# Optimization experiments

Measured on AMD Instinct MI355X. Metric: run time of the kernel, lower is better.

The kernel has to match this reference:

```python
import jax, jax.numpy as jnp
import numpy as np

B, P, D, F = 2048, 16, 1024, 512  # batch, n_prompt, dim, fusion_dim
S = 2 * P  # sequence length
H = D // 2  # classifier hidden
LN_EPS = 1e-5


def _ln_relu(y, g, b):
    mu = jnp.mean(y, axis=-1, keepdims=True)
    var = jnp.mean(jnp.square(y - mu), axis=-1, keepdims=True)
    return jax.nn.relu((y - mu) * jax.lax.rsqrt(var + LN_EPS) * g + b)


def setup_inputs() -> dict:
    key = jax.random.key(0)
    ks = jax.random.split(key, 24)
    n = lambda k, shp, scale: jax.random.normal(k, shp, dtype=jnp.float32) * scale
    return {
        "q": n(ks[0], (B, S, D), 1.0),
        # nn.MultiheadAttention (1 head, batch_first)
        "in_proj_w": n(ks[1], (3 * D, D), 1.0 / np.sqrt(D)),
        "in_proj_b": jnp.zeros((3 * D,), jnp.float32),
        "out_w": n(ks[2], (D, D), 1.0 / np.sqrt(D)),
        "out_b": jnp.zeros((D,), jnp.float32),
        # 32 per-position classifiers, stacked: Linear(D,H)+ReLU+Linear(H,1)+ReLU
        "cls_w1": n(ks[3], (S, H, D), 1.0 / np.sqrt(D)),
        "cls_b1": jnp.zeros((S, H), jnp.float32),
        "cls_w2": n(ks[4], (S, H), 1.0 / np.sqrt(H)),
        "cls_b2": jnp.zeros((S,), jnp.float32),
        # fusion / projector heads: Linear(D,F)+LayerNorm(F)+ReLU
        "fus_w": n(ks[5], (F, D), 1.0 / np.sqrt(D)),
        "fus_b": jnp.zeros((F,), jnp.float32),
        "fus_g": jnp.ones((F,), jnp.float32),
        "fus_be": jnp.zeros((F,), jnp.float32),
        "pa_w": n(ks[6], (F, D), 1.0 / np.sqrt(D)),
        "pa_b": jnp.zeros((F,), jnp.float32),
        "pa_g": jnp.ones((F,), jnp.float32),
        "pa_be": jnp.zeros((F,), jnp.float32),
        "pv_w": n(ks[7], (F, D), 1.0 / np.sqrt(D)),
        "pv_b": jnp.zeros((F,), jnp.float32),
        "pv_g": jnp.ones((F,), jnp.float32),
        "pv_be": jnp.zeros((F,), jnp.float32),
    }


def reference(q, in_proj_w, in_proj_b, out_w, out_b,
              cls_w1, cls_b1, cls_w2, cls_b2,
              fus_w, fus_b, fus_g, fus_be,
              pa_w, pa_b, pa_g, pa_be,
              pv_w, pv_b, pv_g, pv_be):
    # --- single-head self-attention (nn.MultiheadAttention, eval mode) ---
    wq, wk, wv = jnp.split(in_proj_w, 3, axis=0)
    bq, bk, bv = jnp.split(in_proj_b, 3, axis=0)
    qp = jnp.einsum('bsd,ed->bse', q, wq) + bq
    kp = jnp.einsum('bsd,ed->bse', q, wk) + bk
    vp = jnp.einsum('bsd,ed->bse', q, wv) + bv
    scores = jnp.einsum('bse,bte->bst', qp, kp) / jnp.sqrt(jnp.float32(D))
    attn = jax.nn.softmax(scores, axis=-1)
    q_att = jnp.einsum('bst,bte->bse', attn, vp)
    q_att = jnp.einsum('bse,de->bsd', q_att, out_w) + out_b

    # --- per-position tiny classifiers, batched over the 32 slots ---
    h = jax.nn.relu(jnp.einsum('bsd,shd->bsh', q, cls_w1) + cls_b1)  # [B,S,H]
    d = jax.nn.relu(jnp.einsum('bsh,sh->bs', h, cls_w2) + cls_b2)    # [B,S]

    d_a = jax.nn.softmax(d[:, :P], axis=-1)
    d_v = jax.nn.softmax(d[:, P:], axis=-1)
    audio = jnp.einsum('bsd,bs->bd', q_att[:, :P, :], d_a)
    video = jnp.einsum('bsd,bs->bd', q_att[:, P:, :], d_v)
    fusion = (audio + video) * 0.5

    fusion_h = _ln_relu(fusion @ fus_w.T + fus_b, fus_g, fus_be)
    fusion_a = _ln_relu(audio @ pa_w.T + pa_b, pa_g, pa_be)
    fusion_v = _ln_relu(video @ pv_w.T + pv_b, pv_g, pv_be)
    return (fusion_h, fusion_a, fusion_v, d_a, d_v)
```

## Files before the change

kernel.cpp:

```cpp
#include <hip/hip_runtime.h>

#define Bdim 2048
#define Sdim 32
#define Ddim 1024
#define Fdim 512
#define Hdim 512

typedef __bf16 bf16_t;
typedef __bf16 bf16x8 __attribute__((ext_vector_type(8)));
typedef __bf16 bf16x4 __attribute__((ext_vector_type(4)));
typedef float  f32x4  __attribute__((ext_vector_type(4)));

#define BM 128
#define BN 128
#define BK 32

__device__ __forceinline__ void gll16(const bf16_t* g, bf16_t* l) {
  __builtin_amdgcn_global_load_lds((const __attribute__((address_space(1))) void*)g,
                                   (__attribute__((address_space(3))) void*)l,
                                   16, 0, 0);
}

__global__ void k_cvt(const float* __restrict__ s, bf16_t* __restrict__ d, long n) {
  long i = ((long)blockIdx.x * blockDim.x + threadIdx.x) * 4;
  long stride = (long)gridDim.x * blockDim.x * 4;
  for (; i < n; i += stride) {
    float4 v = *(const float4*)(s + i);
    bf16x4 o;
    o[0] = (bf16_t)v.x; o[1] = (bf16_t)v.y; o[2] = (bf16_t)v.z; o[3] = (bf16_t)v.w;
    *(bf16x4*)(d + i) = o;
  }
}

__global__ void k_bias_pre(const float* __restrict__ ipw, const float* __restrict__ ipb,
                           const float* __restrict__ ow, const float* __restrict__ ob,
                           float* __restrict__ u, float* __restrict__ w,
                           float* __restrict__ bp, float* __restrict__ c0) {
  int blk = blockIdx.x, tid = threadIdx.x;
  if (blk < 4) {
    int d = blk * 256 + tid;
    float acc = 0.f;
    for (int e = 0; e < Ddim; ++e) acc += ipw[(long)e * Ddim + d] * ipb[Ddim + e];
    u[d] = acc;
  } else if (blk < 8) {
    int d = (blk - 4) * 256 + tid;
    float acc = 0.f;
    for (int e = 0; e < Ddim; ++e) acc += ipw[(long)(Ddim + e) * Ddim + d] * ipb[e];
    w[d] = acc;
  } else if (blk < 136) {
    int o = (blk - 8) * 8 + (tid >> 5);
    int l = tid & 31;
    float acc = 0.f;
    for (int e = l; e < Ddim; e += 32) acc += ow[(long)o * Ddim + e] * ipb[2 * Ddim + e];
    #pragma unroll
    for (int m = 1; m < 32; m <<= 1) acc += __shfl_xor(acc, m);
    if (l == 0) bp[o] = acc + ob[o];
  } else {
    __shared__ float red[256];
    float acc = 0.f;
    for (int e = tid; e < Ddim; e += 256) acc += ipb[e] * ipb[Ddim + e];
    red[tid] = acc;
    __syncthreads();
    for (int off = 128; off; off >>= 1) {
      if (tid < off) red[tid] += red[tid + off];
      __syncthreads();
    }
    if (tid == 0) c0[0] = red[0];
  }
}

template<int AT, int BT>
__device__ __forceinline__ void gemm_tile(const bf16_t* __restrict__ A, long lda,
                                          const bf16_t* __restrict__ Bt, long ldb,
                                          long m0, long n0, int K,
                                          bf16_t* sa, bf16_t* sb, f32x4 acc[4][4]) {
  const int tid  = threadIdx.x;
  const int wave = tid >> 6;
  const int lane = tid & 63;
  const int quad = lane >> 4;
  const int l16  = lane & 15;
  const int wm = (wave & 1) * 64;
  const int wn = (wave >> 1) * 64;

  for (int kt = 0; kt < K; kt += BK) {
    __syncthreads();
    if constexpr (AT == 0) {
      #pragma unroll
      for (int r = 0; r < 2; ++r) {
        int L = r * 256 + tid;
        const bf16_t* g = A + (m0 + (L >> 2)) * lda + kt + (L & 3) * 8;
        gll16(g, sa + (long)(r * 256 + wave * 64) * 8);
      }
    } else {
      #pragma unroll
      for (int r = 0; r < 2; ++r) {
        int L = r * 256 + tid;
        int gk = L >> 4, gm = (L & 15) * 8;
        bf16x8 v = *(const bf16x8*)(A + (long)(kt + gk) * lda + m0 + gm);
        #pragma unroll
        for (int j = 0; j < 8; ++j) sa[(gm + j) * BK + gk] = v[j];
      }
    }
    if constexpr (BT == 0) {
      #pragma unroll
      for (int r = 0; r < 2; ++r) {
        int L = r * 256 + tid;
        const bf16_t* g = Bt + (n0 + (L >> 2)) * ldb + kt + (L & 3) * 8;
        gll16(g, sb + (long)(r * 256 + wave * 64) * 8);
      }
    } else {
      #pragma unroll
      for (int r = 0; r < 2; ++r) {
        int L = r * 256 + tid;
        int gk = L >> 4, gn = (L & 15) * 8;
        bf16x8 v = *(const bf16x8*)(Bt + (long)(kt + gk) * ldb + n0 + gn);
        #pragma unroll
        for (int j = 0; j < 8; ++j) sb[(gn + j) * BK + gk] = v[j];
      }
    }
    __syncthreads();
    bf16x8 af[4], bfr[4];
    #pragma unroll
    for (int i = 0; i < 4; ++i)
      af[i] = *(const bf16x8*)(sa + (wm + i * 16 + l16) * BK + quad * 8);
    #pragma unroll
    for (int j = 0; j < 4; ++j)
      bfr[j] = *(const bf16x8*)(sb + (wn + j * 16 + l16) * BK + quad * 8);
    #pragma unroll
    for (int i = 0; i < 4; ++i)
      #pragma unroll
      for (int j = 0; j < 4; ++j)
        acc[i][j] = __builtin_amdgcn_mfma_f32_16x16x32_bf16(af[i], bfr[j], acc[i][j], 0, 0, 0);
  }
}

template<int AT, int BT>
__global__ __launch_bounds__(256) void k_gemm_bf16(
    const bf16_t* __restrict__ A, long lda, long sAz,
    const bf16_t* __restrict__ Bt, long ldb, long sBz,
    bf16_t* __restrict__ C, long ldc, long sCz,
    const float* __restrict__ bias, int K) {
  __shared__ bf16_t sa[BM * BK];
  __shared__ bf16_t sb[BN * BK];
  long n0 = (long)blockIdx.x * BN;
  long m0 = (long)blockIdx.y * BM;
  long z  = blockIdx.z;
  const bf16_t* Az = A + z * sAz;
  const bf16_t* Bz = Bt + z * sBz;
  bf16_t* Cz = C + z * sCz;
  f32x4 acc[4][4];
  #pragma unroll
  for (int i = 0; i < 4; ++i)
    #pragma unroll
    for (int j = 0; j < 4; ++j) acc[i][j] = (f32x4){0.f, 0.f, 0.f, 0.f};
  gemm_tile<AT, BT>(Az, lda, Bz, ldb, m0, n0, K, sa, sb, acc);
  const int tid = threadIdx.x, wave = tid >> 6, lane = tid & 63;
  const int quad = lane >> 4, l16 = lane & 15;
  const int wm = (wave & 1) * 64, wn = (wave >> 1) * 64;
  #pragma unroll
  for (int j = 0; j < 4; ++j) {
    long col = n0 + wn + j * 16 + l16;
    float bv = bias ? bias[col] : 0.f;
    #pragma unroll
    for (int i = 0; i < 4; ++i)
      #pragma unroll
      for (int r = 0; r < 4; ++r) {
        long row = m0 + wm + i * 16 + quad * 4 + r;
        Cz[row * ldc + col] = (bf16_t)(acc[i][j][r] + bv);
      }
  }
}

__global__ __launch_bounds__(256) void k_gemm_f32(
    const bf16_t* __restrict__ A, long lda, long sAz,
    const bf16_t* __restrict__ Bt, long ldb, long sBz,
    float* __restrict__ C, long ldc, long sCz, int K) {
  __shared__ bf16_t sa[BM * BK];
  __shared__ bf16_t sb[BN * BK];
  long n0 = (long)blockIdx.x * BN;
  long m0 = (long)blockIdx.y * BM;
  long z  = blockIdx.z;
  const bf16_t* Az = A + z * sAz;
  const bf16_t* Bz = Bt + z * sBz;
  float* Cz = C + z * sCz;
  f32x4 acc[4][4];
  #pragma unroll
  for (int i = 0; i < 4; ++i)
    #pragma unroll
    for (int j = 0; j < 4; ++j) acc[i][j] = (f32x4){0.f, 0.f, 0.f, 0.f};
  gemm_tile<0, 0>(Az, lda, Bz, ldb, m0, n0, K, sa, sb, acc);
  const int tid = threadIdx.x, wave = tid >> 6, lane = tid & 63;
  const int quad = lane >> 4, l16 = lane & 15;
  const int wm = (wave & 1) * 64, wn = (wave >> 1) * 64;
  #pragma unroll
  for (int j = 0; j < 4; ++j) {
    long col = n0 + wn + j * 16 + l16;
    #pragma unroll
    for (int i = 0; i < 4; ++i)
      #pragma unroll
      for (int r = 0; r < 4; ++r) {
        long row = m0 + wm + i * 16 + quad * 4 + r;
        Cz[row * ldc + col] = acc[i][j][r];
      }
  }
}

__global__ __launch_bounds__(256) void k_gemm_cls(
    const bf16_t* __restrict__ q16, const bf16_t* __restrict__ w1,
    const float* __restrict__ b1, const float* __restrict__ w2,
    float* __restrict__ dsum) {
  __shared__ bf16_t sa[BM * BK];
  __shared__ bf16_t sb[BN * BK];
  int s = blockIdx.z;
  long n0 = (long)blockIdx.x * BN;
  long m0 = (long)blockIdx.y * BM;
  const bf16_t* A  = q16 + (long)s * Ddim;
  const bf16_t* Bt = w1 + (long)s * Hdim * Ddim;
  f32x4 acc[4][4];
  #pragma unroll
  for (int i = 0; i < 4; ++i)
    #pragma unroll
    for (int j = 0; j < 4; ++j) acc[i][j] = (f32x4){0.f, 0.f, 0.f, 0.f};
  gemm_tile<0, 0>(A, (long)Sdim * Ddim, Bt, Ddim, m0, n0, Ddim, sa, sb, acc);
  const int tid = threadIdx.x, wave = tid >> 6, lane = tid & 63;
  const int quad = lane >> 4, l16 = lane & 15;
  const int wm = (wave & 1) * 64, wn = (wave >> 1) * 64;
  float b1v[4], w2v[4];
  #pragma unroll
  for (int j = 0; j < 4; ++j) {
    long col = n0 + wn + j * 16 + l16;
    b1v[j] = b1[(long)s * Hdim + col];
    w2v[j] = w2[(long)s * Hdim + col];
  }
  #pragma unroll
  for (int i = 0; i < 4; ++i)
    #pragma unroll
    for (int r = 0; r < 4; ++r) {
      float v = 0.f;
      #pragma unroll
      for (int j = 0; j < 4; ++j) v += fmaxf(acc[i][j][r] + b1v[j], 0.f) * w2v[j];
      v += __shfl_xor(v, 1);
      v += __shfl_xor(v, 2);
      v += __shfl_xor(v, 4);
      v += __shfl_xor(v, 8);
      if (l16 == 0) {
        long row = m0 + wm + i * 16 + quad * 4 + r;
        atomicAdd(&dsum[row * Sdim + s], v);
      }
    }
}

__global__ void k_finalize_d(const float* __restrict__ dsum, const float* __restrict__ cb2,
                             float* __restrict__ daws, float* __restrict__ out_da,
                             float* __restrict__ out_dv) {
  int t = blockIdx.x * 256 + threadIdx.x;
  int b = t >> 5, s = t & 31;
  float v = fmaxf(dsum[t] + cb2[s], 0.f);
  float m = v;
  #pragma unroll
  for (int mask = 1; mask < 16; mask <<= 1) m = fmaxf(m, __shfl_xor(m, mask));
  float e = __expf(v - m);
  float sum = e;
  #pragma unroll
  for (int mask = 1; mask < 16; mask <<= 1) sum += __shfl_xor(sum, mask);
  float r = e / sum;
  daws[t] = r;
  if (s < 16) out_da[b * 16 + s] = r;
  else        out_dv[b * 16 + (s - 16)] = r;
}

#define QPAD 264
__global__ __launch_bounds__(256) void k_attn_pool(
    const bf16_t* __restrict__ q16, const bf16_t* __restrict__ G16,
    const float* __restrict__ daws, const float* __restrict__ u,
    const float* __restrict__ wv, const float* __restrict__ c0p,
    bf16_t* __restrict__ pooled) {
  __shared__ bf16_t qc[32 * QPAD];
  __shared__ bf16_t gc[32 * QPAD];
  __shared__ float sc[32][33];
  __shared__ float qup[32][8], qwp[32][8];
  __shared__ float quL[32], qwL[32], caL[32], cvL[32], daL[16], dvL[16];
  const int tid = threadIdx.x, wave = tid >> 6, lane = tid & 63;
  const int quad = lane >> 4, l16 = lane & 15;
  const long b = blockIdx.x;
  const bf16_t* qb = q16 + b * (Sdim * Ddim);
  const bf16_t* gb = G16 + b * (Sdim * Ddim);
  if (tid < 32) {
    float dval = daws[b * Sdim + tid];
    if (tid < 16) daL[tid] = dval; else dvL[tid - 16] = dval;
  }
  qup[tid >> 3][tid & 7] = 0.f;
  qwp[tid >> 3][tid & 7] = 0.f;
  const int ti = wave & 1, tj = wave >> 1;
  f32x4 acc = (f32x4){0.f, 0.f, 0.f, 0.f};
  for (int kc = 0; kc < Ddim; kc += 256) {
    __syncthreads();
    #pragma unroll
    for (int r = 0; r < 4; ++r) {
      int L = r * 256 + tid;
      int row = L >> 5, koff = (L & 31) * 8;
      *(bf16x8*)(qc + row * QPAD + koff) = *(const bf16x8*)(qb + (long)row * Ddim + kc + koff);
      *(bf16x8*)(gc + row * QPAD + koff) = *(const bf16x8*)(gb + (long)row * Ddim + kc + koff);
    }
    __syncthreads();
    #pragma unroll
    for (int kk = 0; kk < 8; ++kk) {
      bf16x8 a  = *(const bf16x8*)(gc + (ti * 16 + l16) * QPAD + kk * 32 + quad * 8);
      bf16x8 bb = *(const bf16x8*)(qc + (tj * 16 + l16) * QPAD + kk * 32 + quad * 8);
      acc = __builtin_amdgcn_mfma_f32_16x16x32_bf16(a, bb, acc, 0, 0, 0);
    }
    {
      int s2 = tid & 31, sl = tid >> 5;
      float pu = 0.f, pw = 0.f;
      const bf16_t* qrow = qc + s2 * QPAD + sl * 32;
      for (int k = 0; k < 32; ++k) {
        float qv = (float)qrow[k];
        pu += qv * u[kc + sl * 32 + k];
        pw += qv * wv[kc + sl * 32 + k];
      }
      qup[s2][sl] += pu;
      qwp[s2][sl] += pw;
    }
  }
  __syncthreads();
  if (tid < 32) {
    float a0 = 0.f, a1 = 0.f;
    for (int k = 0; k < 8; ++k) { a0 += qup[tid][k]; a1 += qwp[tid][k]; }
    quL[tid] = a0; qwL[tid] = a1;
  }
  __syncthreads();
  {
    float c00 = c0p[0];
    int col = tj * 16 + l16;
    #pragma unroll
    for (int r = 0; r < 4; ++r) {
      int row = ti * 16 + quad * 4 + r;
      sc[row][col] = (acc[r] + quL[row] + qwL[col] + c00) * 0.03125f;
    }
  }
  __syncthreads();
  if (tid < 32) {
    float mx = -1e30f;
    for (int t = 0; t < 32; ++t) mx = fmaxf(mx, sc[tid][t]);
    float sum = 0.f;
    for (int t = 0; t < 32; ++t) { float e = __expf(sc[tid][t] - mx); sc[tid][t] = e; sum += e; }
    float inv = 1.f / sum;
    for (int t = 0; t < 32; ++t) sc[tid][t] *= inv;
  }
  __syncthreads();
  if (tid < 32) {
    float a0 = 0.f, a1 = 0.f;
    for (int s2 = 0; s2 < 16; ++s2) a0 += daL[s2] * sc[s2][tid];
    for (int s2 = 0; s2 < 16; ++s2) a1 += dvL[s2] * sc[16 + s2][tid];
    caL[tid] = a0; cvL[tid] = a1;
  }
  __syncthreads();
  for (int d = tid; d < Ddim; d += 256) {
    float ap = 0.f, vp = 0.f;
    for (int t = 0; t < 32; ++t) {
      float qv = (float)qb[(long)t * Ddim + d];
      ap += caL[t] * qv;
      vp += cvL[t] * qv;
    }
    pooled[b * 3072 + d]        = (bf16_t)(0.5f * (ap + vp));
    pooled[b * 3072 + 1024 + d] = (bf16_t)ap;
    pooled[b * 3072 + 2048 + d] = (bf16_t)vp;
  }
}

__global__ __launch_bounds__(256) void k_ln(
    const float* __restrict__ Y,
    const float* __restrict__ fb, const float* __restrict__ fg, const float* __restrict__ fbe,
    const float* __restrict__ ab, const float* __restrict__ ag, const float* __restrict__ abe,
    const float* __restrict__ vb, const float* __restrict__ vg, const float* __restrict__ vbe,
    float* __restrict__ out) {
  int wave = threadIdx.x >> 6, lane = threadIdx.x & 63;
  long row = (long)blockIdx.x * 4 + wave;
  int head = (int)(row >> 11);
  const float* bb = (head == 0) ? fb : (head == 1) ? ab : vb;
  const float* gg = (head == 0) ? fg : (head == 1) ? ag : vg;
  const float* be = (head == 0) ? fbe : (head == 1) ? abe : vbe;
  const float* y = Y + row * Fdim + lane * 8;
  float v[8];
  float s = 0.f;
  #pragma unroll
  for (int k = 0; k < 8; ++k) { v[k] = y[k] + bb[lane * 8 + k]; s += v[k]; }
  #pragma unroll
  for (int m = 1; m < 64; m <<= 1) s += __shfl_xor(s, m);
  float mu = s * (1.f / Fdim);
  float vs = 0.f;
  #pragma unroll
  for (int k = 0; k < 8; ++k) { float t = v[k] - mu; vs += t * t; }
  #pragma unroll
  for (int m = 1; m < 64; m <<= 1) vs += __shfl_xor(vs, m);
  float inv = rsqrtf(vs * (1.f / Fdim) + 1e-5f);
  float* o = out + row * Fdim + lane * 8;
  #pragma unroll
  for (int k = 0; k < 8; ++k) {
    float t = (v[k] - mu) * inv * gg[lane * 8 + k] + be[lane * 8 + k];
    o[k] = fmaxf(t, 0.f);
  }
}

extern "C" void kernel_launch(void* const* d_in, const int* in_sizes, int n_in,
                              void* d_out, int out_size, void* d_ws, size_t ws_size,
                              hipStream_t stream) {
  const float* q    = (const float*)d_in[0];
  const float* ipw  = (const float*)d_in[1];
  const float* ipb  = (const float*)d_in[2];
  const float* ow   = (const float*)d_in[3];
  const float* ob   = (const float*)d_in[4];
  const float* cw1  = (const float*)d_in[5];
  const float* cb1  = (const float*)d_in[6];
  const float* cw2  = (const float*)d_in[7];
  const float* cb2  = (const float*)d_in[8];
  const float* fusw = (const float*)d_in[9];
  const float* fusb = (const float*)d_in[10];
  const float* fusg = (const float*)d_in[11];
  const float* fusbe= (const float*)d_in[12];
  const float* paw  = (const float*)d_in[13];
  const float* pab  = (const float*)d_in[14];
  const float* pag  = (const float*)d_in[15];
  const float* pabe = (const float*)d_in[16];
  const float* pvw  = (const float*)d_in[17];
  const float* pvb  = (const float*)d_in[18];
  const float* pvg  = (const float*)d_in[19];
  const float* pvbe = (const float*)d_in[20];
  float* out = (float*)d_out;

  const size_t o_q16   = 0;
  const size_t o_w16   = 134217728;
  const size_t o_ow16  = 140509184;
  const size_t o_cls16 = 142606336;
  const size_t o_hw16  = 176160768;
  const size_t o_Mt    = 179306496;
  const size_t o_Nt    = 181403648;
  const size_t o_G16   = 183500800;
  const size_t o_pool  = 317718528;
  const size_t o_u     = 330301440;
  const size_t o_wv    = 330305536;
  const size_t o_bp    = 330309632;
  const size_t o_c0    = 330313728;
  const size_t o_dsum  = 330313984;
  const size_t o_daws  = 330576128;
  const size_t total   = 330838272;
  if (ws_size < total) return;

  char* ws = (char*)d_ws;
  bf16_t* q16   = (bf16_t*)(ws + o_q16);
  bf16_t* w16   = (bf16_t*)(ws + o_w16);
  bf16_t* Wq16  = w16;
  bf16_t* Wk16  = w16 + 1048576;
  bf16_t* Wv16  = w16 + 2097152;
  bf16_t* ow16  = (bf16_t*)(ws + o_ow16);
  bf16_t* cls16 = (bf16_t*)(ws + o_cls16);
  bf16_t* hw16  = (bf16_t*)(ws + o_hw16);
  bf16_t* Mt    = (bf16_t*)(ws + o_Mt);
  bf16_t* Nt    = (bf16_t*)(ws + o_Nt);
  bf16_t* G16   = (bf16_t*)(ws + o_G16);
  bf16_t* S116  = (bf16_t*)(ws + o_G16);
  float*  Yf    = (float*)(ws + o_G16 + 12582912);
  bf16_t* pool16= (bf16_t*)(ws + o_pool);
  float*  uf    = (float*)(ws + o_u);
  float*  wvf   = (float*)(ws + o_wv);
  float*  bpf   = (float*)(ws + o_bp);
  float*  c0f   = (float*)(ws + o_c0);
  float*  dsum  = (float*)(ws + o_dsum);
  float*  daws  = (float*)(ws + o_daws);

  auto cvt = [&](const float* s, bf16_t* d, long n) {
    long blocks = (n / 4 + 255) / 256;
    if (blocks > 8192) blocks = 8192;
    k_cvt<<<dim3((unsigned)blocks), dim3(256), 0, stream>>>(s, d, n);
  };

  cvt(q,    q16,   (long)Bdim * Sdim * Ddim);
  cvt(ipw,  w16,   3L * Ddim * Ddim);
  cvt(ow,   ow16,  (long)Ddim * Ddim);
  cvt(cw1,  cls16, (long)Sdim * Hdim * Ddim);
  cvt(fusw, hw16,            (long)Fdim * Ddim);
  cvt(paw,  hw16 + 524288,   (long)Fdim * Ddim);
  cvt(pvw,  hw16 + 1048576,  (long)Fdim * Ddim);

  k_bias_pre<<<dim3(137), dim3(256), 0, stream>>>(ipw, ipb, ow, ob, uf, wvf, bpf, c0f);

  k_gemm_bf16<1, 1><<<dim3(8, 8, 1), dim3(256), 0, stream>>>(
      Wk16, Ddim, 0, Wq16, Ddim, 0, Mt, Ddim, 0, nullptr, Ddim);

  k_gemm_bf16<0, 1><<<dim3(8, 8, 1), dim3(256), 0, stream>>>(
      ow16, Ddim, 0, Wv16, Ddim, 0, Nt, Ddim, 0, nullptr, Ddim);

  k_gemm_bf16<0, 0><<<dim3(8, 512, 1), dim3(256), 0, stream>>>(
      q16, Ddim, 0, Mt, Ddim, 0, G16, Ddim, 0, nullptr, Ddim);

  hipMemsetAsync(dsum, 0, (size_t)Bdim * Sdim * sizeof(float), stream);
  k_gemm_cls<<<dim3(4, 16, 32), dim3(256), 0, stream>>>(q16, cls16, cb1, cw2, dsum);

  k_finalize_d<<<dim3(256), dim3(256), 0, stream>>>(
      dsum, cb2, daws, out + 3145728, out + 3145728 + 32768);

  k_attn_pool<<<dim3(2048), dim3(256), 0, stream>>>(q16, G16, daws, uf, wvf, c0f, pool16);

  k_gemm_bf16<0, 0><<<dim3(8, 48, 1), dim3(256), 0, stream>>>(
      pool16, Ddim, 0, Nt, Ddim, 0, S116, Ddim, 0, bpf, Ddim);

  k_gemm_f32<<<dim3(4, 16, 3), dim3(256), 0, stream>>>(
      S116, 3L * Ddim, Ddim, hw16, Ddim, (long)Fdim * Ddim,
      Yf, Fdim, (long)Bdim * Fdim, Ddim);

  k_ln<<<dim3(1536), dim3(256), 0, stream>>>(
      Yf, fusb, fusg, fusbe, pab, pag, pabe, pvb, pvg, pvbe, out);
}
```

Measured before the change: 1.129 ms.

## Add 128x256 big GEMM, swap MFMA operands for vector stores, fuse conversions

Merges the seven fp32-to-bf16 conversion launches into one kernel. Swaps the MFMA operand order so each lane holds four consecutive columns, which lets the GEMM epilogues write vectorised bf16x4/f32x4 stores and lets the classifier reduction use two cross-quad shuffles. Adds a dedicated 128x256-tile GEMM with XCD-aware block remapping for the large q·M product. Also remaps classifier blocks for locality and vectorises the attention-pool loads and stores. Risks: the larger tile raises register pressure, and the remapping index math must stay exact.

```diff
diff --git a/kernel.cpp b/kernel.cpp
--- a/kernel.cpp
+++ b/kernel.cpp
@@ -21,15 +21,27 @@
                                    16, 0, 0);
 }
 
-__global__ void k_cvt(const float* __restrict__ s, bf16_t* __restrict__ d, long n) {
-  long i = ((long)blockIdx.x * blockDim.x + threadIdx.x) * 4;
-  long stride = (long)gridDim.x * blockDim.x * 4;
-  for (; i < n; i += stride) {
-    float4 v = *(const float4*)(s + i);
-    bf16x4 o;
-    o[0] = (bf16_t)v.x; o[1] = (bf16_t)v.y; o[2] = (bf16_t)v.z; o[3] = (bf16_t)v.w;
-    *(bf16x4*)(d + i) = o;
-  }
+__global__ void k_cvt_all(const float* __restrict__ q, const float* __restrict__ ipw,
+                          const float* __restrict__ ow, const float* __restrict__ cw1,
+                          const float* __restrict__ fusw, const float* __restrict__ paw,
+                          const float* __restrict__ pvw,
+                          bf16_t* __restrict__ q16, bf16_t* __restrict__ w16,
+                          bf16_t* __restrict__ ow16, bf16_t* __restrict__ cls16,
+                          bf16_t* __restrict__ hw16) {
+  long v = (long)blockIdx.x * 256 + threadIdx.x;
+  const float* s; bf16_t* d; long off;
+  if (v < 16777216L)      { s = q;    d = q16;            off = 0; }
+  else if (v < 17563648L) { s = ipw;  d = w16;            off = 16777216L; }
+  else if (v < 17825792L) { s = ow;   d = ow16;           off = 17563648L; }
+  else if (v < 22020096L) { s = cw1;  d = cls16;          off = 17825792L; }
+  else if (v < 22151168L) { s = fusw; d = hw16;           off = 22020096L; }
+  else if (v < 22282240L) { s = paw;  d = hw16 + 524288;  off = 22151168L; }
+  else                    { s = pvw;  d = hw16 + 1048576; off = 22282240L; }
+  long i = (v - off) * 4;
+  float4 t = *(const float4*)(s + i);
+  bf16x4 o;
+  o[0] = (bf16_t)t.x; o[1] = (bf16_t)t.y; o[2] = (bf16_t)t.z; o[3] = (bf16_t)t.w;
+  *(bf16x4*)(d + i) = o;
 }
 
 __global__ void k_bias_pre(const float* __restrict__ ipw, const float* __restrict__ ipb,
@@ -130,7 +142,7 @@
     for (int i = 0; i < 4; ++i)
       #pragma unroll
       for (int j = 0; j < 4; ++j)
-        acc[i][j] = __builtin_amdgcn_mfma_f32_16x16x32_bf16(af[i], bfr[j], acc[i][j], 0, 0, 0);
+        acc[i][j] = __builtin_amdgcn_mfma_f32_16x16x32_bf16(bfr[j], af[i], acc[i][j], 0, 0, 0);
   }
 }
 
@@ -158,16 +170,17 @@
   const int quad = lane >> 4, l16 = lane & 15;
   const int wm = (wave & 1) * 64, wn = (wave >> 1) * 64;
   #pragma unroll
-  for (int j = 0; j < 4; ++j) {
-    long col = n0 + wn + j * 16 + l16;
-    float bv = bias ? bias[col] : 0.f;
-    #pragma unroll
-    for (int i = 0; i < 4; ++i)
-      #pragma unroll
-      for (int r = 0; r < 4; ++r) {
-        long row = m0 + wm + i * 16 + quad * 4 + r;
-        Cz[row * ldc + col] = (bf16_t)(acc[i][j][r] + bv);
-      }
+  for (int i = 0; i < 4; ++i) {
+    long row = m0 + wm + i * 16 + l16;
+    #pragma unroll
+    for (int j = 0; j < 4; ++j) {
+      long col = n0 + wn + j * 16 + quad * 4;
+      f32x4 b4 = bias ? *(const f32x4*)(bias + col) : (f32x4){0.f, 0.f, 0.f, 0.f};
+      bf16x4 o;
+      #pragma unroll
+      for (int r = 0; r < 4; ++r) o[r] = (bf16_t)(acc[i][j][r] + b4[r]);
+      *(bf16x4*)(Cz + row * ldc + col) = o;
+    }
   }
 }
 
@@ -193,15 +206,71 @@
   const int quad = lane >> 4, l16 = lane & 15;
   const int wm = (wave & 1) * 64, wn = (wave >> 1) * 64;
   #pragma unroll
-  for (int j = 0; j < 4; ++j) {
-    long col = n0 + wn + j * 16 + l16;
+  for (int i = 0; i < 4; ++i) {
+    long row = m0 + wm + i * 16 + l16;
+    #pragma unroll
+    for (int j = 0; j < 4; ++j) {
+      long col = n0 + wn + j * 16 + quad * 4;
+      *(f32x4*)(Cz + row * ldc + col) = acc[i][j];
+    }
+  }
+}
+
+__global__ __launch_bounds__(256, 2) void k_gemm_big(
+    const bf16_t* __restrict__ A, const bf16_t* __restrict__ Bt,
+    bf16_t* __restrict__ C) {
+  __shared__ bf16_t sa[128 * 32];
+  __shared__ bf16_t sb[256 * 32];
+  const int tid = threadIdx.x, wave = tid >> 6, lane = tid & 63;
+  const int quad = lane >> 4, l16 = lane & 15;
+  int lin = blockIdx.y * 4 + blockIdx.x;
+  int c = lin & 7, j0 = lin >> 3;
+  long m0 = ((long)c * 64 + (j0 >> 2)) * 128;
+  long n0 = (long)(j0 & 3) * 256;
+  const int wm = (wave & 1) * 64;
+  const int wn = (wave >> 1) * 128;
+  f32x4 acc[4][8];
+  #pragma unroll
+  for (int i = 0; i < 4; ++i)
+    #pragma unroll
+    for (int j = 0; j < 8; ++j) acc[i][j] = (f32x4){0.f, 0.f, 0.f, 0.f};
+  for (int kt = 0; kt < 1024; kt += 32) {
+    __syncthreads();
+    #pragma unroll
+    for (int r = 0; r < 2; ++r) {
+      int L = r * 256 + tid;
+      gll16(A + (m0 + (L >> 2)) * 1024 + kt + (L & 3) * 8, sa + (long)(r * 256 + wave * 64) * 8);
+    }
+    #pragma unroll
+    for (int r = 0; r < 4; ++r) {
+      int L = r * 256 + tid;
+      gll16(Bt + (n0 + (L >> 2)) * 1024 + kt + (L & 3) * 8, sb + (long)(r * 256 + wave * 64) * 8);
+    }
+    __syncthreads();
+    bf16x8 af[4], bfr[8];
     #pragma unroll
     for (int i = 0; i < 4; ++i)
-      #pragma unroll
-      for (int r = 0; r < 4; ++r) {
-        long row = m0 + wm + i * 16 + quad * 4 + r;
-        Cz[row * ldc + col] = acc[i][j][r];
-      }
+      af[i] = *(const bf16x8*)(sa + (wm + i * 16 + l16) * 32 + quad * 8);
+    #pragma unroll
+    for (int j = 0; j < 8; ++j)
+      bfr[j] = *(const bf16x8*)(sb + (wn + j * 16 + l16) * 32 + quad * 8);
+    #pragma unroll
+    for (int i = 0; i < 4; ++i)
+      #pragma unroll
+      for (int j = 0; j < 8; ++j)
+        acc[i][j] = __builtin_amdgcn_mfma_f32_16x16x32_bf16(bfr[j], af[i], acc[i][j], 0, 0, 0);
+  }
+  #pragma unroll
+  for (int i = 0; i < 4; ++i) {
+    long row = m0 + wm + i * 16 + l16;
+    #pragma unroll
+    for (int j = 0; j < 8; ++j) {
+      long col = n0 + wn + j * 16 + quad * 4;
+      bf16x4 o;
+      #pragma unroll
+      for (int r = 0; r < 4; ++r) o[r] = (bf16_t)(acc[i][j][r]);
+      *(bf16x4*)(C + row * 1024 + col) = o;
+    }
   }
 }
 
@@ -211,9 +280,12 @@
     float* __restrict__ dsum) {
   __shared__ bf16_t sa[BM * BK];
   __shared__ bf16_t sb[BN * BK];
-  int s = blockIdx.z;
-  long n0 = (long)blockIdx.x * BN;
-  long m0 = (long)blockIdx.y * BM;
+  int lin = ((int)blockIdx.z * 16 + blockIdx.y) * 4 + blockIdx.x;
+  int c = lin & 7, j0 = lin >> 3;
+  int p = c + 8 * (j0 >> 2);
+  long n0 = (long)(j0 & 3) * BN;
+  int s = p >> 4;
+  long m0 = (long)(p & 15) * BM;
   const bf16_t* A  = q16 + (long)s * Ddim;
   const bf16_t* Bt = w1 + (long)s * Hdim * Ddim;
   f32x4 acc[4][4];
@@ -225,29 +297,27 @@
   const int tid = threadIdx.x, wave = tid >> 6, lane = tid & 63;
   const int quad = lane >> 4, l16 = lane & 15;
   const int wm = (wave & 1) * 64, wn = (wave >> 1) * 64;
-  float b1v[4], w2v[4];
-  #pragma unroll
-  for (int j = 0; j < 4; ++j) {
-    long col = n0 + wn + j * 16 + l16;
-    b1v[j] = b1[(long)s * Hdim + col];
-    w2v[j] = w2[(long)s * Hdim + col];
-  }
-  #pragma unroll
-  for (int i = 0; i < 4; ++i)
-    #pragma unroll
-    for (int r = 0; r < 4; ++r) {
-      float v = 0.f;
-      #pragma unroll
-      for (int j = 0; j < 4; ++j) v += fmaxf(acc[i][j][r] + b1v[j], 0.f) * w2v[j];
-      v += __shfl_xor(v, 1);
-      v += __shfl_xor(v, 2);
-      v += __shfl_xor(v, 4);
-      v += __shfl_xor(v, 8);
-      if (l16 == 0) {
-        long row = m0 + wm + i * 16 + quad * 4 + r;
-        atomicAdd(&dsum[row * Sdim + s], v);
-      }
-    }
+  const float* b1s = b1 + (long)s * Hdim;
+  const float* w2s = w2 + (long)s * Hdim;
+  #pragma unroll
+  for (int i = 0; i < 4; ++i) {
+    float vsum = 0.f;
+    #pragma unroll
+    for (int j = 0; j < 4; ++j) {
+      long col = n0 + wn + j * 16 + quad * 4;
+      f32x4 b4 = *(const f32x4*)(b1s + col);
+      f32x4 w4 = *(const f32x4*)(w2s + col);
+      #pragma unroll
+      for (int r = 0; r < 4; ++r)
+        vsum += fmaxf(acc[i][j][r] + b4[r], 0.f) * w4[r];
+    }
+    vsum += __shfl_xor(vsum, 16);
+    vsum += __shfl_xor(vsum, 32);
+    if (lane < 16) {
+      long row = m0 + wm + i * 16 + l16;
+      atomicAdd(&dsum[row * Sdim + s], vsum);
+    }
+  }
 }
 
 __global__ void k_finalize_d(const float* __restrict__ dsum, const float* __restrict__ cb2,
@@ -355,16 +425,29 @@
     caL[tid] = a0; cvL[tid] = a1;
   }
   __syncthreads();
-  for (int d = tid; d < Ddim; d += 256) {
-    float ap = 0.f, vp = 0.f;
+  {
+    int d0 = tid * 4;
+    float ap[4] = {0.f, 0.f, 0.f, 0.f}, vp[4] = {0.f, 0.f, 0.f, 0.f};
     for (int t = 0; t < 32; ++t) {
-      float qv = (float)qb[(long)t * Ddim + d];
-      ap += caL[t] * qv;
-      vp += cvL[t] * qv;
-    }
-    pooled[b * 3072 + d]        = (bf16_t)(0.5f * (ap + vp));
-    pooled[b * 3072 + 1024 + d] = (bf16_t)ap;
-    pooled[b * 3072 + 2048 + d] = (bf16_t)vp;
+      float ca = caL[t], cv = cvL[t];
+      bf16x4 qv = *(const bf16x4*)(qb + (long)t * Ddim + d0);
+      #pragma unroll
+      for (int e = 0; e < 4; ++e) {
+        float x = (float)qv[e];
+        ap[e] += ca * x;
+        vp[e] += cv * x;
+      }
+    }
+    bf16x4 pf, pa, pv;
+    #pragma unroll
+    for (int e = 0; e < 4; ++e) {
+      pf[e] = (bf16_t)(0.5f * (ap[e] + vp[e]));
+      pa[e] = (bf16_t)ap[e];
+      pv[e] = (bf16_t)vp[e];
+    }
+    *(bf16x4*)(pooled + b * 3072 + d0)        = pf;
+    *(bf16x4*)(pooled + b * 3072 + 1024 + d0) = pa;
+    *(bf16x4*)(pooled + b * 3072 + 2048 + d0) = pv;
   }
 }
 
@@ -468,19 +551,8 @@
   float*  dsum  = (float*)(ws + o_dsum);
   float*  daws  = (float*)(ws + o_daws);
 
-  auto cvt = [&](const float* s, bf16_t* d, long n) {
-    long blocks = (n / 4 + 255) / 256;
-    if (blocks > 8192) blocks = 8192;
-    k_cvt<<<dim3((unsigned)blocks), dim3(256), 0, stream>>>(s, d, n);
-  };
-
-  cvt(q,    q16,   (long)Bdim * Sdim * Ddim);
-  cvt(ipw,  w16,   3L * Ddim * Ddim);
-  cvt(ow,   ow16,  (long)Ddim * Ddim);
-  cvt(cw1,  cls16, (long)Sdim * Hdim * Ddim);
-  cvt(fusw, hw16,            (long)Fdim * Ddim);
-  cvt(paw,  hw16 + 524288,   (long)Fdim * Ddim);
-  cvt(pvw,  hw16 + 1048576,  (long)Fdim * Ddim);
+  k_cvt_all<<<dim3(87552), dim3(256), 0, stream>>>(
+      q, ipw, ow, cw1, fusw, paw, pvw, q16, w16, ow16, cls16, hw16);
 
   k_bias_pre<<<dim3(137), dim3(256), 0, stream>>>(ipw, ipb, ow, ob, uf, wvf, bpf, c0f);
 
@@ -490,8 +562,7 @@
   k_gemm_bf16<0, 1><<<dim3(8, 8, 1), dim3(256), 0, stream>>>(
       ow16, Ddim, 0, Wv16, Ddim, 0, Nt, Ddim, 0, nullptr, Ddim);
 
-  k_gemm_bf16<0, 0><<<dim3(8, 512, 1), dim3(256), 0, stream>>>(
-      q16, Ddim, 0, Mt, Ddim, 0, G16, Ddim, 0, nullptr, Ddim);
+  k_gemm_big<<<dim3(4, 512), dim3(256), 0, stream>>>(q16, Mt, G16);
 
   hipMemsetAsync(dsum, 0, (size_t)Bdim * Sdim * sizeof(float), stream);
   k_gemm_cls<<<dim3(4, 16, 32), dim3(256), 0, stream>>>(q16, cls16, cb1, cw2, dsum);
```

Result: faster. 1.058 ms (-6.3%).
